# Performance work log

Hardware: AMD Instinct MI355X
Metric: run time of the kernel (lower is better)

## Reference

```python
import jax, jax.numpy as jnp
import numpy as np

B, S, D, H, A = 2, 2048, 1024, 16, 64
INIT_STD = 0.02


def setup_inputs() -> dict:
    key = jax.random.key(0)
    ks = jax.random.split(key, 5)
    return {
        "residual": jax.random.normal(ks[0], (B, S, D), dtype=jnp.float32),
        "Wq": jax.random.normal(ks[1], (H, D, A), dtype=jnp.float32) * INIT_STD,
        "Wk": jax.random.normal(ks[2], (H, D, A), dtype=jnp.float32) * INIT_STD,
        "Wv": jax.random.normal(ks[3], (H, D, A), dtype=jnp.float32) * INIT_STD,
        "Wo": jax.random.normal(ks[4], (H, A, D), dtype=jnp.float32) * INIT_STD,
        "bq": jnp.zeros((H, A), dtype=jnp.float32),
        "bk": jnp.zeros((H, A), dtype=jnp.float32),
        "bv": jnp.zeros((H, A), dtype=jnp.float32),
        "bo": jnp.zeros((D,), dtype=jnp.float32),
    }


def reference(residual, Wq, Wk, Wv, Wo, bq, bk, bv, bo):
    # residual: [B,S,D]; W{q,k,v}: [H,D,A]; Wo: [H,A,D]
    q = jnp.einsum("bsd,hda->bhsa", residual, Wq) + bq[None, :, None, :]
    k = jnp.einsum("bsd,hda->bhsa", residual, Wk) + bk[None, :, None, :]
    v = jnp.einsum("bsd,hda->bhsa", residual, Wv) + bv[None, :, None, :]
    scale = 1.0 / jnp.sqrt(jnp.float32(q.shape[-1]))
    scores = jnp.einsum("bhsa,bhta->bhst", q, k) * scale  # [B,H,S,S]
    s = scores.shape[-1]
    causal = jnp.tril(jnp.ones((s, s), dtype=bool))  # True = keep
    # original masked_fill with -100000.0 (not -inf); stay faithful
    masked = jnp.where(causal, scores, jnp.float32(-100000.0))
    pattern = jax.nn.softmax(masked, axis=-1)
    z = jnp.einsum("bhst,bhta->bshа".replace("а", "a"), pattern, v)  # [B,S,H,A]
    out = jnp.einsum("bsha,had->bsd", z, Wo) + bo
    return out
```

## Files before the change

kernel.cpp:

```cpp
#include <hip/hip_runtime.h>
#include <hip/hip_bf16.h>

#define B_ 2
#define S_ 2048
#define D_ 1024
#define H_ 16
#define A_ 64

typedef __attribute__((ext_vector_type(8))) short bf16x8;
typedef __attribute__((ext_vector_type(4))) float f32x4;

#define QSCALE 0.1803368801111204f

__device__ inline short f2bf(float f) {
    union { float f; unsigned u; } x; x.f = f;
    unsigned r = x.u + 0x7fff + ((x.u >> 16) & 1);
    return (short)(r >> 16);
}

__global__ __launch_bounds__(256) void cast_kernel(const float* __restrict__ x,
                                                   short* __restrict__ y, int n) {
    int i = (blockIdx.x * 256 + threadIdx.x) * 8;
    if (i < n) {
        float4 a = *(const float4*)(x + i);
        float4 b = *(const float4*)(x + i + 4);
        bf16x8 o;
        o[0]=f2bf(a.x); o[1]=f2bf(a.y); o[2]=f2bf(a.z); o[3]=f2bf(a.w);
        o[4]=f2bf(b.x); o[5]=f2bf(b.y); o[6]=f2bf(b.z); o[7]=f2bf(b.w);
        *(bf16x8*)(y + i) = o;
    }
}

__global__ __launch_bounds__(256) void wtrans_kernel(
    const float* __restrict__ Wq, const float* __restrict__ Wk,
    const float* __restrict__ Wv, const float* __restrict__ Wo,
    short* __restrict__ Wt, short* __restrict__ Wot) {
    const int kt = blockIdx.x, yy = blockIdx.y, z = blockIdx.z;
    __shared__ short T[64 * 72];
    const int tid = threadIdx.x;
    const int r = tid >> 2, c0 = (tid & 3) * 16;
    const float* src;
    if (z < 3) {
        const float* W = z == 0 ? Wq : (z == 1 ? Wk : Wv);
        src = &W[yy * (D_ * A_) + (kt * 64 + r) * A_ + c0];
    } else {
        src = &Wo[(kt * 64 + r) * D_ + yy * 64 + c0];
    }
    #pragma unroll
    for (int q = 0; q < 4; q++) {
        float4 f = *(const float4*)(src + q * 4);
        T[r * 72 + c0 + q * 4 + 0] = f2bf(f.x);
        T[r * 72 + c0 + q * 4 + 1] = f2bf(f.y);
        T[r * 72 + c0 + q * 4 + 2] = f2bf(f.z);
        T[r * 72 + c0 + q * 4 + 3] = f2bf(f.w);
    }
    __syncthreads();
    const int a = tid >> 2, kc = (tid & 3) * 16;
    bf16x8 o0, o1;
    #pragma unroll
    for (int j = 0; j < 8; j++) {
        o0[j] = T[(kc + j) * 72 + a];
        o1[j] = T[(kc + 8 + j) * 72 + a];
    }
    const int n_base = (z < 3) ? z * 1024 + yy * 64 : yy * 64;
    short* dst = (z < 3) ? &Wt[(n_base + a) * D_ + kt * 64 + kc]
                         : &Wot[(n_base + a) * D_ + kt * 64 + kc];
    *(bf16x8*)dst = o0;
    *(bf16x8*)(dst + 8) = o1;
}

__global__ __launch_bounds__(256) void qkv_gemm(
    const short* __restrict__ X, const short* __restrict__ Wt,
    const float* __restrict__ bq, const float* __restrict__ bk, const float* __restrict__ bv,
    short* __restrict__ Qb, short* __restrict__ Kb, short* __restrict__ Vt) {
    const int mt = blockIdx.x, nt = blockIdx.y;
    const int m0 = mt * 128, n0 = nt * 128;
    const int sel = n0 >> 10;
    __shared__ short Xl[2][128 * 40], Wl[2][128 * 40];
    const int tid = threadIdx.x, wv = tid >> 6, lane = tid & 63, quad = lane >> 4, l16 = lane & 15;
    const int grow = tid >> 1, gk = (tid & 1) * 16;
    f32x4 acc[4][4] = {};
    bf16x8 xr0, xr1, wr0, wr1;
    {
        const short* xs = &X[(m0 + grow) * D_ + gk];
        xr0 = *(const bf16x8*)xs; xr1 = *(const bf16x8*)(xs + 8);
        const short* wsp = &Wt[(n0 + grow) * D_ + gk];
        wr0 = *(const bf16x8*)wsp; wr1 = *(const bf16x8*)(wsp + 8);
    }
    const int rm = (wv & 1) * 64, cn = (wv >> 1) * 64;
    for (int i = 0; i < 32; i++) {
        const int bu = i & 1;
        *(bf16x8*)&Xl[bu][grow * 40 + gk]     = xr0;
        *(bf16x8*)&Xl[bu][grow * 40 + gk + 8] = xr1;
        *(bf16x8*)&Wl[bu][grow * 40 + gk]     = wr0;
        *(bf16x8*)&Wl[bu][grow * 40 + gk + 8] = wr1;
        __syncthreads();
        if (i < 31) {
            const int k0 = (i + 1) * 32;
            const short* xs = &X[(m0 + grow) * D_ + k0 + gk];
            xr0 = *(const bf16x8*)xs; xr1 = *(const bf16x8*)(xs + 8);
            const short* wsp = &Wt[(n0 + grow) * D_ + k0 + gk];
            wr0 = *(const bf16x8*)wsp; wr1 = *(const bf16x8*)(wsp + 8);
        }
        bf16x8 af[4];
        #pragma unroll
        for (int rt = 0; rt < 4; rt++)
            af[rt] = *(bf16x8*)&Xl[bu][(rm + rt * 16 + l16) * 40 + quad * 8];
        #pragma unroll
        for (int ct = 0; ct < 4; ct++) {
            bf16x8 bf = *(bf16x8*)&Wl[bu][(cn + ct * 16 + l16) * 40 + quad * 8];
            #pragma unroll
            for (int rt = 0; rt < 4; rt++)
                acc[rt][ct] = __builtin_amdgcn_mfma_f32_16x16x32_bf16(af[rt], bf, acc[rt][ct], 0, 0, 0);
        }
    }
    const int b = m0 >> 11;
    const float* bias = sel == 0 ? bq : (sel == 1 ? bk : bv);
    if (sel < 2) {
        short* dst = sel == 0 ? Qb : Kb;
        const float scale = sel == 0 ? QSCALE : 1.0f;
        #pragma unroll
        for (int ct = 0; ct < 4; ct++) {
            const int n = n0 + cn + ct * 16 + l16;
            const int h = (n >> 6) & 15, a = n & 63;
            const float bi = bias[n & 1023];
            #pragma unroll
            for (int rt = 0; rt < 4; rt++)
                #pragma unroll
                for (int r = 0; r < 4; r++) {
                    const int row = m0 + rm + rt * 16 + quad * 4 + r;
                    const int s = row & (S_ - 1);
                    dst[(((b * H_) + h) * S_ + s) * A_ + a] = f2bf((acc[rt][ct][r] + bi) * scale);
                }
        }
    } else {
        #pragma unroll
        for (int ct = 0; ct < 4; ct++) {
            const int n = n0 + cn + ct * 16 + l16;
            const int h = (n >> 6) & 15, a = n & 63;
            const float bi = bias[n & 1023];
            #pragma unroll
            for (int rt = 0; rt < 4; rt++) {
                short4 pk;
                pk.x = f2bf(acc[rt][ct][0] + bi);
                pk.y = f2bf(acc[rt][ct][1] + bi);
                pk.z = f2bf(acc[rt][ct][2] + bi);
                pk.w = f2bf(acc[rt][ct][3] + bi);
                const int row = m0 + rm + rt * 16 + quad * 4;
                const int s = row & (S_ - 1);
                *(short4*)&Vt[(((b * H_) + h) * A_ + a) * S_ + s] = pk;
            }
        }
    }
}

__global__ __launch_bounds__(256) void flash_kernel(
    const short* __restrict__ Qb, const short* __restrict__ Kb,
    const short* __restrict__ Vt, short* __restrict__ Z) {
    const int p = blockIdx.x, h = blockIdx.y, b = blockIdx.z;
    const int bh = b * H_ + h;
    const int qlo = p, qhi = 31 - p;
    __shared__ short Ql[2][64 * 72], Kl[2][64 * 72], Vl[2][64 * 72], Pl[4][16 * 72];
    const int tid = threadIdx.x, wv = tid >> 6, lane = tid & 63, quad = lane >> 4, l16 = lane & 15;
    const int srow = tid >> 2, sc0 = (tid & 3) * 16;
    #pragma unroll
    for (int t = 0; t < 2; t++) {
        const int qt = t ? qhi : qlo;
        const short* src = &Qb[(bh * S_ + qt * 64 + srow) * A_ + sc0];
        *(bf16x8*)&Ql[t][srow * 72 + sc0]     = *(const bf16x8*)src;
        *(bf16x8*)&Ql[t][srow * 72 + sc0 + 8] = *(const bf16x8*)(src + 8);
    }
    f32x4 O[2][4] = {};
    float m_i[2][4], l_i[2][4];
    #pragma unroll
    for (int t = 0; t < 2; t++)
        #pragma unroll
        for (int r = 0; r < 4; r++) { m_i[t][r] = -1e30f; l_i[t][r] = 0.f; }
    bf16x8 kr0, kr1, vr0, vr1;
    {
        const short* ks = &Kb[(bh * S_ + srow) * A_ + sc0];
        kr0 = *(const bf16x8*)ks; kr1 = *(const bf16x8*)(ks + 8);
        const short* vs = &Vt[(bh * A_ + srow) * S_ + sc0];
        vr0 = *(const bf16x8*)vs; vr1 = *(const bf16x8*)(vs + 8);
    }
    for (int kt = 0; kt <= qhi; kt++) {
        const int bu = kt & 1;
        *(bf16x8*)&Kl[bu][srow * 72 + sc0]     = kr0;
        *(bf16x8*)&Kl[bu][srow * 72 + sc0 + 8] = kr1;
        *(bf16x8*)&Vl[bu][srow * 72 + sc0]     = vr0;
        *(bf16x8*)&Vl[bu][srow * 72 + sc0 + 8] = vr1;
        __syncthreads();
        if (kt < qhi) {
            const short* ks = &Kb[(bh * S_ + (kt + 1) * 64 + srow) * A_ + sc0];
            kr0 = *(const bf16x8*)ks; kr1 = *(const bf16x8*)(ks + 8);
            const short* vs = &Vt[(bh * A_ + srow) * S_ + (kt + 1) * 64 + sc0];
            vr0 = *(const bf16x8*)vs; vr1 = *(const bf16x8*)(vs + 8);
        }
        const int nt_upd = (kt <= qlo) ? 2 : 1;
        for (int u = 0; u < nt_upd; u++) {
            const int t = (u == 0) ? 1 : 0;
            const int qt = t ? qhi : qlo;
            f32x4 sacc[4];
            #pragma unroll
            for (int ct = 0; ct < 4; ct++) {
                f32x4 acc = {};
                #pragma unroll
                for (int kk = 0; kk < 2; kk++) {
                    bf16x8 a  = *(bf16x8*)&Ql[t][(wv * 16 + l16) * 72 + kk * 32 + quad * 8];
                    bf16x8 bb = *(bf16x8*)&Kl[bu][(ct * 16 + l16) * 72 + kk * 32 + quad * 8];
                    acc = __builtin_amdgcn_mfma_f32_16x16x32_bf16(a, bb, acc, 0, 0, 0);
                }
                sacc[ct] = acc;
            }
            if (kt == qt) {
                #pragma unroll
                for (int ct = 0; ct < 4; ct++) {
                    const int cl = ct * 16 + l16;
                    #pragma unroll
                    for (int r = 0; r < 4; r++) {
                        const int rl = wv * 16 + quad * 4 + r;
                        if (cl > rl) sacc[ct][r] = -1e30f;
                    }
                }
            }
            #pragma unroll
            for (int r = 0; r < 4; r++) {
                float v = fmaxf(fmaxf(sacc[0][r], sacc[1][r]), fmaxf(sacc[2][r], sacc[3][r]));
                #pragma unroll
                for (int mm = 1; mm < 16; mm <<= 1) v = fmaxf(v, __shfl_xor(v, mm));
                const float mn = fmaxf(m_i[t][r], v);
                const float alpha = exp2f(m_i[t][r] - mn);
                float rs = 0.f;
                #pragma unroll
                for (int ct = 0; ct < 4; ct++) {
                    const float pe = exp2f(sacc[ct][r] - mn);
                    sacc[ct][r] = pe; rs += pe;
                }
                l_i[t][r] = l_i[t][r] * alpha + rs;
                m_i[t][r] = mn;
                #pragma unroll
                for (int ct = 0; ct < 4; ct++) O[t][ct][r] *= alpha;
            }
            short* Pw = &Pl[wv][0];
            #pragma unroll
            for (int ct = 0; ct < 4; ct++)
                #pragma unroll
                for (int r = 0; r < 4; r++)
                    Pw[(quad * 4 + r) * 72 + ct * 16 + l16] = f2bf(sacc[ct][r]);
            __builtin_amdgcn_s_waitcnt(0xC07F);
            #pragma unroll
            for (int ct = 0; ct < 4; ct++) {
                #pragma unroll
                for (int kk = 0; kk < 2; kk++) {
                    bf16x8 a  = *(bf16x8*)&Pw[l16 * 72 + kk * 32 + quad * 8];
                    bf16x8 bb = *(bf16x8*)&Vl[bu][(ct * 16 + l16) * 72 + kk * 32 + quad * 8];
                    O[t][ct] = __builtin_amdgcn_mfma_f32_16x16x32_bf16(a, bb, O[t][ct], 0, 0, 0);
                }
            }
        }
    }
    #pragma unroll
    for (int t = 0; t < 2; t++) {
        const int qt = t ? qhi : qlo;
        float lsum[4];
        #pragma unroll
        for (int r = 0; r < 4; r++) {
            float rs = l_i[t][r];
            #pragma unroll
            for (int mm = 1; mm < 16; mm <<= 1) rs += __shfl_xor(rs, mm);
            lsum[r] = rs;
        }
        #pragma unroll
        for (int ct = 0; ct < 4; ct++) {
            const int a = ct * 16 + l16;
            #pragma unroll
            for (int r = 0; r < 4; r++) {
                const int s = qt * 64 + wv * 16 + quad * 4 + r;
                Z[(b * S_ + s) * (H_ * A_) + h * A_ + a] = f2bf(O[t][ct][r] / lsum[r]);
            }
        }
    }
}

__global__ __launch_bounds__(256) void proj_gemm(
    const short* __restrict__ Zb, const short* __restrict__ Wot,
    const float* __restrict__ bo, float* __restrict__ out) {
    const int mt = blockIdx.x, nt = blockIdx.y;
    const int m0 = mt * 128, n0 = nt * 128;
    __shared__ short Xl[2][128 * 40], Wl[2][128 * 40];
    const int tid = threadIdx.x, wv = tid >> 6, lane = tid & 63, quad = lane >> 4, l16 = lane & 15;
    const int grow = tid >> 1, gk = (tid & 1) * 16;
    f32x4 acc[4][4] = {};
    bf16x8 xr0, xr1, wr0, wr1;
    {
        const short* xs = &Zb[(m0 + grow) * D_ + gk];
        xr0 = *(const bf16x8*)xs; xr1 = *(const bf16x8*)(xs + 8);
        const short* wsp = &Wot[(n0 + grow) * D_ + gk];
        wr0 = *(const bf16x8*)wsp; wr1 = *(const bf16x8*)(wsp + 8);
    }
    const int rm = (wv & 1) * 64, cn = (wv >> 1) * 64;
    for (int i = 0; i < 32; i++) {
        const int bu = i & 1;
        *(bf16x8*)&Xl[bu][grow * 40 + gk]     = xr0;
        *(bf16x8*)&Xl[bu][grow * 40 + gk + 8] = xr1;
        *(bf16x8*)&Wl[bu][grow * 40 + gk]     = wr0;
        *(bf16x8*)&Wl[bu][grow * 40 + gk + 8] = wr1;
        __syncthreads();
        if (i < 31) {
            const int k0 = (i + 1) * 32;
            const short* xs = &Zb[(m0 + grow) * D_ + k0 + gk];
            xr0 = *(const bf16x8*)xs; xr1 = *(const bf16x8*)(xs + 8);
            const short* wsp = &Wot[(n0 + grow) * D_ + k0 + gk];
            wr0 = *(const bf16x8*)wsp; wr1 = *(const bf16x8*)(wsp + 8);
        }
        bf16x8 af[4];
        #pragma unroll
        for (int rt = 0; rt < 4; rt++)
            af[rt] = *(bf16x8*)&Xl[bu][(rm + rt * 16 + l16) * 40 + quad * 8];
        #pragma unroll
        for (int ct = 0; ct < 4; ct++) {
            bf16x8 bf = *(bf16x8*)&Wl[bu][(cn + ct * 16 + l16) * 40 + quad * 8];
            #pragma unroll
            for (int rt = 0; rt < 4; rt++)
                acc[rt][ct] = __builtin_amdgcn_mfma_f32_16x16x32_bf16(af[rt], bf, acc[rt][ct], 0, 0, 0);
        }
    }
    #pragma unroll
    for (int ct = 0; ct < 4; ct++) {
        const int n = n0 + cn + ct * 16 + l16;
        const float bi = bo[n];
        #pragma unroll
        for (int rt = 0; rt < 4; rt++)
            #pragma unroll
            for (int r = 0; r < 4; r++) {
                const int row = m0 + rm + rt * 16 + quad * 4 + r;
                out[row * D_ + n] = acc[rt][ct][r] + bi;
            }
    }
}

extern "C" void kernel_launch(void* const* d_in, const int* in_sizes, int n_in,
                              void* d_out, int out_size, void* d_ws, size_t ws_size,
                              hipStream_t stream) {
    const float* residual = (const float*)d_in[0];
    const float* Wq = (const float*)d_in[1];
    const float* Wk = (const float*)d_in[2];
    const float* Wv = (const float*)d_in[3];
    const float* Wo = (const float*)d_in[4];
    const float* bq = (const float*)d_in[5];
    const float* bk = (const float*)d_in[6];
    const float* bv = (const float*)d_in[7];
    const float* bo = (const float*)d_in[8];
    float* out = (float*)d_out;

    char* ws = (char*)d_ws;
    const size_t NE = (size_t)B_ * S_ * D_;
    short* Xbf = (short*)(ws);
    short* Wt  = (short*)(ws +  8ull * 1024 * 1024);
    short* Wot = (short*)(ws + 14ull * 1024 * 1024);
    short* Qb  = (short*)(ws + 16ull * 1024 * 1024);
    short* Kb  = (short*)(ws + 24ull * 1024 * 1024);
    short* Vt  = (short*)(ws + 32ull * 1024 * 1024);
    short* Zb  = (short*)(ws + 40ull * 1024 * 1024);

    hipLaunchKernelGGL(cast_kernel, dim3((int)(NE / (256 * 8))), dim3(256), 0, stream,
                       residual, Xbf, (int)NE);
    hipLaunchKernelGGL(wtrans_kernel, dim3(16, 16, 4), dim3(256), 0, stream,
                       Wq, Wk, Wv, Wo, Wt, Wot);
    hipLaunchKernelGGL(qkv_gemm, dim3(32, 24), dim3(256), 0, stream,
                       Xbf, Wt, bq, bk, bv, Qb, Kb, Vt);
    hipLaunchKernelGGL(flash_kernel, dim3(16, H_, B_), dim3(256), 0, stream,
                       Qb, Kb, Vt, Zb);
    hipLaunchKernelGGL(proj_gemm, dim3(32, 8), dim3(256), 0, stream,
                       Zb, Wot, bo, out);
}
```

Measured before the change: 222.9 us.

## Load Q/K/V fragments directly from global into registers, drop LDS staging and barriers

```diff
diff --git a/kernel.cpp b/kernel.cpp
--- a/kernel.cpp
+++ b/kernel.cpp
@@ -16,6 +16,31 @@
     union { float f; unsigned u; } x; x.f = f;
     unsigned r = x.u + 0x7fff + ((x.u >> 16) & 1);
     return (short)(r >> 16);
+}
+
+__device__ inline float dpp_max16(float x) {
+    int v;
+    v = __builtin_amdgcn_update_dpp(0, __builtin_bit_cast(int, x), 0xB1, 0xF, 0xF, false);
+    x = fmaxf(x, __builtin_bit_cast(float, v));
+    v = __builtin_amdgcn_update_dpp(0, __builtin_bit_cast(int, x), 0x4E, 0xF, 0xF, false);
+    x = fmaxf(x, __builtin_bit_cast(float, v));
+    v = __builtin_amdgcn_update_dpp(0, __builtin_bit_cast(int, x), 0x141, 0xF, 0xF, false);
+    x = fmaxf(x, __builtin_bit_cast(float, v));
+    v = __builtin_amdgcn_update_dpp(0, __builtin_bit_cast(int, x), 0x140, 0xF, 0xF, false);
+    x = fmaxf(x, __builtin_bit_cast(float, v));
+    return x;
+}
+__device__ inline float dpp_sum16(float x) {
+    int v;
+    v = __builtin_amdgcn_update_dpp(0, __builtin_bit_cast(int, x), 0xB1, 0xF, 0xF, false);
+    x += __builtin_bit_cast(float, v);
+    v = __builtin_amdgcn_update_dpp(0, __builtin_bit_cast(int, x), 0x4E, 0xF, 0xF, false);
+    x += __builtin_bit_cast(float, v);
+    v = __builtin_amdgcn_update_dpp(0, __builtin_bit_cast(int, x), 0x141, 0xF, 0xF, false);
+    x += __builtin_bit_cast(float, v);
+    v = __builtin_amdgcn_update_dpp(0, __builtin_bit_cast(int, x), 0x140, 0xF, 0xF, false);
+    x += __builtin_bit_cast(float, v);
+    return x;
 }
 
 __global__ __launch_bounds__(256) void cast_kernel(const float* __restrict__ x,
@@ -154,132 +179,113 @@
     }
 }
 
-__global__ __launch_bounds__(256) void flash_kernel(
+__global__ __launch_bounds__(256, 4) void flash_kernel(
     const short* __restrict__ Qb, const short* __restrict__ Kb,
     const short* __restrict__ Vt, short* __restrict__ Z) {
     const int p = blockIdx.x, h = blockIdx.y, b = blockIdx.z;
     const int bh = b * H_ + h;
     const int qlo = p, qhi = 31 - p;
-    __shared__ short Ql[2][64 * 72], Kl[2][64 * 72], Vl[2][64 * 72], Pl[4][16 * 72];
+    __shared__ short Pl[4][16 * 72];
     const int tid = threadIdx.x, wv = tid >> 6, lane = tid & 63, quad = lane >> 4, l16 = lane & 15;
-    const int srow = tid >> 2, sc0 = (tid & 3) * 16;
+    short* Pw = &Pl[wv][0];
+
+    bf16x8 qf0[2], qf1[2];
+    {
+        const short* q0 = &Qb[(bh * S_ + qlo * 64 + wv * 16 + l16) * A_ + quad * 8];
+        qf0[0] = *(const bf16x8*)q0; qf0[1] = *(const bf16x8*)(q0 + 32);
+        const short* q1 = &Qb[(bh * S_ + qhi * 64 + wv * 16 + l16) * A_ + quad * 8];
+        qf1[0] = *(const bf16x8*)q1; qf1[1] = *(const bf16x8*)(q1 + 32);
+    }
+    f32x4 O0[4] = {}, O1[4] = {};
+    float m0[4], l0[4], m1[4], l1[4];
     #pragma unroll
-    for (int t = 0; t < 2; t++) {
-        const int qt = t ? qhi : qlo;
-        const short* src = &Qb[(bh * S_ + qt * 64 + srow) * A_ + sc0];
-        *(bf16x8*)&Ql[t][srow * 72 + sc0]     = *(const bf16x8*)src;
-        *(bf16x8*)&Ql[t][srow * 72 + sc0 + 8] = *(const bf16x8*)(src + 8);
-    }
-    f32x4 O[2][4] = {};
-    float m_i[2][4], l_i[2][4];
-    #pragma unroll
-    for (int t = 0; t < 2; t++)
-        #pragma unroll
-        for (int r = 0; r < 4; r++) { m_i[t][r] = -1e30f; l_i[t][r] = 0.f; }
-    bf16x8 kr0, kr1, vr0, vr1;
-    {
-        const short* ks = &Kb[(bh * S_ + srow) * A_ + sc0];
-        kr0 = *(const bf16x8*)ks; kr1 = *(const bf16x8*)(ks + 8);
-        const short* vs = &Vt[(bh * A_ + srow) * S_ + sc0];
-        vr0 = *(const bf16x8*)vs; vr1 = *(const bf16x8*)(vs + 8);
-    }
+    for (int r = 0; r < 4; r++) { m0[r] = -1e30f; l0[r] = 0.f; m1[r] = -1e30f; l1[r] = 0.f; }
+
+    auto do_update = [&](const bf16x8 (&qf)[2], f32x4 (&O)[4], float (&m_i)[4],
+                         float (&l_i)[4], int qt, int kt) {
+        const short* kbase = &Kb[(bh * S_ + kt * 64 + l16) * A_ + quad * 8];
+        f32x4 sacc[4];
+        #pragma unroll
+        for (int ct = 0; ct < 4; ct++) {
+            const short* kp = kbase + ct * 16 * A_;
+            bf16x8 k0 = *(const bf16x8*)kp;
+            bf16x8 k1 = *(const bf16x8*)(kp + 32);
+            f32x4 acc = {};
+            acc = __builtin_amdgcn_mfma_f32_16x16x32_bf16(qf[0], k0, acc, 0, 0, 0);
+            acc = __builtin_amdgcn_mfma_f32_16x16x32_bf16(qf[1], k1, acc, 0, 0, 0);
+            sacc[ct] = acc;
+        }
+        if (kt == qt) {
+            #pragma unroll
+            for (int ct = 0; ct < 4; ct++) {
+                const int cl = ct * 16 + l16;
+                #pragma unroll
+                for (int r = 0; r < 4; r++) {
+                    const int rl = wv * 16 + quad * 4 + r;
+                    if (cl > rl) sacc[ct][r] = -1e30f;
+                }
+            }
+        }
+        #pragma unroll
+        for (int r = 0; r < 4; r++) {
+            float v = fmaxf(fmaxf(sacc[0][r], sacc[1][r]), fmaxf(sacc[2][r], sacc[3][r]));
+            v = dpp_max16(v);
+            const float mn = fmaxf(m_i[r], v);
+            const float alpha = exp2f(m_i[r] - mn);
+            float rs = 0.f;
+            #pragma unroll
+            for (int ct = 0; ct < 4; ct++) {
+                const float pe = exp2f(sacc[ct][r] - mn);
+                sacc[ct][r] = pe; rs += pe;
+            }
+            l_i[r] = l_i[r] * alpha + rs;
+            m_i[r] = mn;
+            #pragma unroll
+            for (int ct = 0; ct < 4; ct++) O[ct][r] *= alpha;
+        }
+        bf16x8 vf[4][2];
+        #pragma unroll
+        for (int ct = 0; ct < 4; ct++) {
+            const short* vp = &Vt[(bh * A_ + ct * 16 + l16) * S_ + kt * 64 + quad * 8];
+            vf[ct][0] = *(const bf16x8*)vp;
+            vf[ct][1] = *(const bf16x8*)(vp + 32);
+        }
+        #pragma unroll
+        for (int ct = 0; ct < 4; ct++)
+            #pragma unroll
+            for (int r = 0; r < 4; r++)
+                Pw[(quad * 4 + r) * 72 + ct * 16 + l16] = f2bf(sacc[ct][r]);
+        __builtin_amdgcn_s_waitcnt(0xC07F);
+        bf16x8 pa0 = *(bf16x8*)&Pw[l16 * 72 + quad * 8];
+        bf16x8 pa1 = *(bf16x8*)&Pw[l16 * 72 + 32 + quad * 8];
+        #pragma unroll
+        for (int ct = 0; ct < 4; ct++) {
+            O[ct] = __builtin_amdgcn_mfma_f32_16x16x32_bf16(pa0, vf[ct][0], O[ct], 0, 0, 0);
+            O[ct] = __builtin_amdgcn_mfma_f32_16x16x32_bf16(pa1, vf[ct][1], O[ct], 0, 0, 0);
+        }
+    };
+
     for (int kt = 0; kt <= qhi; kt++) {
-        const int bu = kt & 1;
-        *(bf16x8*)&Kl[bu][srow * 72 + sc0]     = kr0;
-        *(bf16x8*)&Kl[bu][srow * 72 + sc0 + 8] = kr1;
-        *(bf16x8*)&Vl[bu][srow * 72 + sc0]     = vr0;
-        *(bf16x8*)&Vl[bu][srow * 72 + sc0 + 8] = vr1;
-        __syncthreads();
-        if (kt < qhi) {
-            const short* ks = &Kb[(bh * S_ + (kt + 1) * 64 + srow) * A_ + sc0];
-            kr0 = *(const bf16x8*)ks; kr1 = *(const bf16x8*)(ks + 8);
-            const short* vs = &Vt[(bh * A_ + srow) * S_ + (kt + 1) * 64 + sc0];
-            vr0 = *(const bf16x8*)vs; vr1 = *(const bf16x8*)(vs + 8);
-        }
-        const int nt_upd = (kt <= qlo) ? 2 : 1;
-        for (int u = 0; u < nt_upd; u++) {
-            const int t = (u == 0) ? 1 : 0;
-            const int qt = t ? qhi : qlo;
-            f32x4 sacc[4];
-            #pragma unroll
-            for (int ct = 0; ct < 4; ct++) {
-                f32x4 acc = {};
-                #pragma unroll
-                for (int kk = 0; kk < 2; kk++) {
-                    bf16x8 a  = *(bf16x8*)&Ql[t][(wv * 16 + l16) * 72 + kk * 32 + quad * 8];
-                    bf16x8 bb = *(bf16x8*)&Kl[bu][(ct * 16 + l16) * 72 + kk * 32 + quad * 8];
-                    acc = __builtin_amdgcn_mfma_f32_16x16x32_bf16(a, bb, acc, 0, 0, 0);
-                }
-                sacc[ct] = acc;
-            }
-            if (kt == qt) {
-                #pragma unroll
-                for (int ct = 0; ct < 4; ct++) {
-                    const int cl = ct * 16 + l16;
-                    #pragma unroll
-                    for (int r = 0; r < 4; r++) {
-                        const int rl = wv * 16 + quad * 4 + r;
-                        if (cl > rl) sacc[ct][r] = -1e30f;
-                    }
-                }
-            }
-            #pragma unroll
-            for (int r = 0; r < 4; r++) {
-                float v = fmaxf(fmaxf(sacc[0][r], sacc[1][r]), fmaxf(sacc[2][r], sacc[3][r]));
-                #pragma unroll
-                for (int mm = 1; mm < 16; mm <<= 1) v = fmaxf(v, __shfl_xor(v, mm));
-                const float mn = fmaxf(m_i[t][r], v);
-                const float alpha = exp2f(m_i[t][r] - mn);
-                float rs = 0.f;
-                #pragma unroll
-                for (int ct = 0; ct < 4; ct++) {
-                    const float pe = exp2f(sacc[ct][r] - mn);
-                    sacc[ct][r] = pe; rs += pe;
-                }
-                l_i[t][r] = l_i[t][r] * alpha + rs;
-                m_i[t][r] = mn;
-                #pragma unroll
-                for (int ct = 0; ct < 4; ct++) O[t][ct][r] *= alpha;
-            }
-            short* Pw = &Pl[wv][0];
-            #pragma unroll
-            for (int ct = 0; ct < 4; ct++)
-                #pragma unroll
-                for (int r = 0; r < 4; r++)
-                    Pw[(quad * 4 + r) * 72 + ct * 16 + l16] = f2bf(sacc[ct][r]);
-            __builtin_amdgcn_s_waitcnt(0xC07F);
-            #pragma unroll
-            for (int ct = 0; ct < 4; ct++) {
-                #pragma unroll
-                for (int kk = 0; kk < 2; kk++) {
-                    bf16x8 a  = *(bf16x8*)&Pw[l16 * 72 + kk * 32 + quad * 8];
-                    bf16x8 bb = *(bf16x8*)&Vl[bu][(ct * 16 + l16) * 72 + kk * 32 + quad * 8];
-                    O[t][ct] = __builtin_amdgcn_mfma_f32_16x16x32_bf16(a, bb, O[t][ct], 0, 0, 0);
-                }
-            }
-        }
-    }
-    #pragma unroll
-    for (int t = 0; t < 2; t++) {
-        const int qt = t ? qhi : qlo;
+        do_update(qf1, O1, m1, l1, qhi, kt);
+        if (kt <= qlo) do_update(qf0, O0, m0, l0, qlo, kt);
+    }
+
+    auto epilogue = [&](f32x4 (&O)[4], float (&l_i)[4], int qt) {
         float lsum[4];
         #pragma unroll
-        for (int r = 0; r < 4; r++) {
-            float rs = l_i[t][r];
-            #pragma unroll
-            for (int mm = 1; mm < 16; mm <<= 1) rs += __shfl_xor(rs, mm);
-            lsum[r] = rs;
-        }
+        for (int r = 0; r < 4; r++) lsum[r] = dpp_sum16(l_i[r]);
         #pragma unroll
         for (int ct = 0; ct < 4; ct++) {
             const int a = ct * 16 + l16;
             #pragma unroll
             for (int r = 0; r < 4; r++) {
                 const int s = qt * 64 + wv * 16 + quad * 4 + r;
-                Z[(b * S_ + s) * (H_ * A_) + h * A_ + a] = f2bf(O[t][ct][r] / lsum[r]);
-            }
-        }
-    }
+                Z[(b * S_ + s) * (H_ * A_) + h * A_ + a] = f2bf(O[ct][r] / lsum[r]);
+            }
+        }
+    };
+    epilogue(O1, l1, qhi);
+    epilogue(O0, l0, qlo);
 }
 
 __global__ __launch_bounds__(256) void proj_gemm(
```

Result: slower. 304.1 us (+36.5%).
